# Optimization experiments

Measured on AMD Instinct MI355X. Metric: run time of the kernel, lower is better.

The kernel has to match this reference:

```python
import jax, jax.numpy as jnp
import numpy as np

EMBED_DIM = 1024
NUM_HEADS = 16
HEAD_DIM = EMBED_DIM // NUM_HEADS


def setup_inputs() -> dict:
    key = jax.random.key(0)
    ks = jax.random.split(key, 5)
    x = jax.random.normal(ks[0], (2, 2048, EMBED_DIM), dtype=jnp.float32)
    s_in = 1.0 / np.sqrt(EMBED_DIM)
    W_qkv = jax.random.uniform(ks[1], (EMBED_DIM, 3 * EMBED_DIM), minval=-s_in, maxval=s_in, dtype=jnp.float32)
    b_qkv = jax.random.uniform(ks[2], (3 * EMBED_DIM,), minval=-s_in, maxval=s_in, dtype=jnp.float32)
    W_out = jax.random.uniform(ks[3], (EMBED_DIM, EMBED_DIM), minval=-s_in, maxval=s_in, dtype=jnp.float32)
    b_out = jax.random.uniform(ks[4], (EMBED_DIM,), minval=-s_in, maxval=s_in, dtype=jnp.float32)
    return {"x": x, "W_qkv": W_qkv, "b_qkv": b_qkv, "W_out": W_out, "b_out": b_out}


def reference(x, W_qkv, b_qkv, W_out, b_out):
    B, S, D = x.shape
    H, Dh = NUM_HEADS, HEAD_DIM
    qkv = x @ W_qkv + b_qkv                       # [B, S, 3D]
    q, k, v = jnp.split(qkv, 3, axis=-1)
    # [B, S, D] -> [B, H, S, Dh]
    q = q.reshape(B, S, H, Dh).transpose(0, 2, 1, 3)
    k = k.reshape(B, S, H, Dh).transpose(0, 2, 1, 3)
    v = v.reshape(B, S, H, Dh).transpose(0, 2, 1, 3)
    scores = jnp.einsum('bhqd,bhkd->bhqk', q, k) / jnp.sqrt(jnp.float32(Dh))
    probs = jax.nn.softmax(scores, axis=-1)       # [B, H, S, S]
    attn = jnp.einsum('bhqk,bhkd->bhqd', probs, v)
    attn = attn.transpose(0, 2, 1, 3).reshape(B, S, D)
    return attn @ W_out + b_out
```

## Files before the change

kernel.cpp:

```cpp
#include <hip/hip_runtime.h>
#include <hip/hip_bf16.h>

#define DEV __device__ __forceinline__

typedef __bf16 bf16x8 __attribute__((ext_vector_type(8)));
typedef float f32x4 __attribute__((ext_vector_type(4)));
typedef float f32x16 __attribute__((ext_vector_type(16)));
using u16 = unsigned short;
using u32 = unsigned int;

static constexpr int S = 2048;
static constexpr int D = 1024;
static constexpr float SCQ = 0.125f * 1.44269504088896340736f;

DEV u16 f2bf(float f) {
  unsigned u = __builtin_bit_cast(unsigned, f);
  u += 0x7fffu + ((u >> 16) & 1u);
  return (u16)(u >> 16);
}
DEV u16 f2bfr(float f) {
  return (u16)((__builtin_bit_cast(u32, f) + 0x8000u) >> 16);
}
DEV u32 pk2(float a, float b) {
  u32 ua = __builtin_bit_cast(u32, a) + 0x8000u;
  u32 ub = __builtin_bit_cast(u32, b) + 0x8000u;
  return __builtin_amdgcn_perm(ub, ua, 0x07060302);
}

DEV void gl16(const u16* __restrict__ g, u16* l) {
  __builtin_amdgcn_global_load_lds((const __attribute__((address_space(1))) u32*)g,
                                   (__attribute__((address_space(3))) u32*)l, 16, 0, 0);
}

__global__ __launch_bounds__(256) void k_prep(const float* __restrict__ x, u16* __restrict__ Xb,
                                              const float* __restrict__ Wqkv, u16* __restrict__ WqkvT,
                                              const float* __restrict__ Wout, u16* __restrict__ WoutT) {
  __shared__ float t[32][33];
  const int bid = blockIdx.x;
  const int tid = threadIdx.x;
  if (bid < 4096) {
    const int i = bid * 256 + tid;
    const float4 v = reinterpret_cast<const float4*>(x)[i];
    ushort4 o;
    o.x = f2bf(v.x); o.y = f2bf(v.y); o.z = f2bf(v.z); o.w = f2bf(v.w);
    reinterpret_cast<ushort4*>(Xb)[i] = o;
    return;
  }
  const float* in;
  u16* out;
  int R, C, bx, by;
  if (bid < 4096 + 3072) {
    const int b = bid - 4096;
    in = Wqkv; out = WqkvT; R = 1024; C = 3072;
    bx = b % 96; by = b / 96;
  } else {
    const int b = bid - 7168;
    in = Wout; out = WoutT; R = 1024; C = 1024;
    bx = b & 31; by = b >> 5;
  }
  const int tx = tid & 31, ty = tid >> 5;
  const int c0 = bx * 32, r0 = by * 32;
  for (int i = ty; i < 32; i += 8)
    t[i][tx] = in[(size_t)(r0 + i) * C + c0 + tx];
  __syncthreads();
  for (int i = ty; i < 32; i += 8)
    out[(size_t)(c0 + i) * R + r0 + tx] = f2bf(t[tx][i]);
}

__global__ __launch_bounds__(256, 5) void k_gemm0(const u16* __restrict__ A, const u16* __restrict__ Bt,
                                                  const float* __restrict__ bias, int M, int N, int K,
                                                  u16* __restrict__ Qb, u16* __restrict__ Kb,
                                                  u16* __restrict__ Vt) {
  constexpr int TN = 128, NJ = 4;
  constexpr int ASZ = 2 * 128 * 32 * 2;
  __shared__ __align__(16) char smem[ASZ + 2 * TN * 32 * 2];
  auto As = reinterpret_cast<u16(*)[128][32]>(smem);
  auto Bs = reinterpret_cast<u16(*)[TN][32]>(smem + ASZ);
  auto LT = reinterpret_cast<u16(*)[136]>(smem);
  const int tid = threadIdx.x;
  const int lane = tid & 63, wave = tid >> 6;
  const int l15 = lane & 15, quad = lane >> 4;
  const int bid0 = blockIdx.x + 24 * blockIdx.y;
  const int bid = (bid0 & 7) * 96 + (bid0 >> 3);
  const int m0 = (bid / 24) * 128, n0 = (bid % 24) * TN;
  const int wm = (wave >> 1) * 64, wn = (wave & 1) * (TN / 2);
  const int lr = lane >> 2;
  const int lcs = ((((lane & 3) - (lane >> 3)) & 3)) * 8;
  const int sq = ((quad + (l15 >> 1)) & 3) * 8;

  f32x4 acc[4][NJ];
#pragma unroll
  for (int i = 0; i < 4; i++)
#pragma unroll
    for (int j = 0; j < NJ; j++) acc[i][j] = (f32x4){0.f, 0.f, 0.f, 0.f};

  const u16* Aw0 = &A[(size_t)(m0 + wave * 32 + lr) * K + lcs];
  const u16* Aw1 = &A[(size_t)(m0 + wave * 32 + 16 + lr) * K + lcs];
  const u16* Bw0 = &Bt[(size_t)(n0 + wave * 32 + lr) * K + lcs];
  const u16* Bw1 = &Bt[(size_t)(n0 + wave * 32 + 16 + lr) * K + lcs];

  gl16(Aw0, &As[0][wave * 32][0]);
  gl16(Aw1, &As[0][wave * 32 + 16][0]);
  gl16(Bw0, &Bs[0][wave * 32][0]);
  gl16(Bw1, &Bs[0][wave * 32 + 16][0]);

  int cur = 0;
#pragma unroll 2
  for (int kk = 0; kk < K; kk += 32, cur ^= 1) {
    __syncthreads();
    if (kk + 32 < K) {
      gl16(Aw0 + kk + 32, &As[cur ^ 1][wave * 32][0]);
      gl16(Aw1 + kk + 32, &As[cur ^ 1][wave * 32 + 16][0]);
      gl16(Bw0 + kk + 32, &Bs[cur ^ 1][wave * 32][0]);
      gl16(Bw1 + kk + 32, &Bs[cur ^ 1][wave * 32 + 16][0]);
    }
    bf16x8 af[4], bfv[NJ];
#pragma unroll
    for (int i = 0; i < 4; i++)
      af[i] = *reinterpret_cast<const bf16x8*>(&As[cur][wm + i * 16 + l15][sq]);
#pragma unroll
    for (int j = 0; j < NJ; j++)
      bfv[j] = *reinterpret_cast<const bf16x8*>(&Bs[cur][wn + j * 16 + l15][sq]);
#pragma unroll
    for (int i = 0; i < 4; i++)
#pragma unroll
      for (int j = 0; j < NJ; j++)
        acc[i][j] = __builtin_amdgcn_mfma_f32_16x16x32_bf16(af[i], bfv[j], acc[i][j], 0, 0, 0);
  }

  if (n0 >= 2048) {
    const int b = m0 >> 11, sbase = m0 & 2047;
#pragma unroll
    for (int p = 0; p < 2; p++) {
      __syncthreads();
      if ((wave & 1) == p) {
#pragma unroll
        for (int j = 0; j < NJ; j++) {
          const int n = n0 + wn + j * 16 + l15;
          const float vb = bias[n];
#pragma unroll
          for (int i = 0; i < 4; i++) {
            uint2 pw;
            pw.x = pk2(acc[i][j][0] + vb, acc[i][j][1] + vb);
            pw.y = pk2(acc[i][j][2] + vb, acc[i][j][3] + vb);
            *reinterpret_cast<uint2*>(&LT[j * 16 + l15][wm + i * 16 + quad * 4]) = pw;
          }
        }
      }
      __syncthreads();
      const int h = ((n0 - 2048) >> 6) + p;
      const int bh = b * 16 + h;
      const int nl = tid >> 2, cc = (tid & 3) * 32;
      u16* dst = &Vt[((size_t)bh * 64 + nl) * S + sbase + cc];
#pragma unroll
      for (int k = 0; k < 4; k++)
        reinterpret_cast<uint4*>(dst)[k] = *reinterpret_cast<const uint4*>(&LT[nl][cc + k * 8]);
    }
  } else {
#pragma unroll
    for (int i = 0; i < 4; i++) {
#pragma unroll
      for (int j = 0; j < NJ; j++) {
#pragma unroll
        for (int r = 0; r < 4; r++) {
          const int m = m0 + wm + i * 16 + quad * 4 + r;
          const int n = n0 + wn + j * 16 + l15;
          const float v = acc[i][j][r] + bias[n];
          const int h = (n >> 6) & 15, dh = n & 63;
          const int b = m >> 11, s = m & 2047;
          const int bh = b * 16 + h;
          if (n < 1024) Qb[((size_t)bh * S + s) * 64 + dh] = f2bfr(v * SCQ);
          else          Kb[((size_t)bh * S + s) * 64 + dh] = f2bfr(v);
        }
      }
    }
  }
}

__global__ __launch_bounds__(256, 4) void k_gemm2(const u16* __restrict__ A, const u16* __restrict__ Bt,
                                                  const float* __restrict__ bias, float* __restrict__ outF) {
  constexpr int K = 1024, N = 1024;
  __shared__ __align__(16) u16 As[2][64][64];
  __shared__ __align__(16) u16 Bs[2][64][64];
  const int tid = threadIdx.x;
  const int lane = tid & 63, wave = tid >> 6;
  const int l15 = lane & 15, quad = lane >> 4;
  const int bid0 = blockIdx.x + 16 * blockIdx.y;
  const int bid = (bid0 & 7) * 128 + (bid0 >> 3);
  const int m0 = (bid >> 4) * 64, n0 = (bid & 15) * 64;
  const int wm = (wave >> 1) * 32, wn = (wave & 1) * 32;
  const int srow = lane >> 3;
  const int scol = ((lane & 7) ^ srow) * 8;

  f32x4 acc[2][2];
#pragma unroll
  for (int i = 0; i < 2; i++)
#pragma unroll
    for (int j = 0; j < 2; j++) acc[i][j] = (f32x4){0.f, 0.f, 0.f, 0.f};

  const u16* Ap[2];
  const u16* Bp[2];
#pragma unroll
  for (int c = 0; c < 2; c++) {
    Ap[c] = &A[(size_t)(m0 + wave * 16 + c * 8 + srow) * K + scol];
    Bp[c] = &Bt[(size_t)(n0 + wave * 16 + c * 8 + srow) * K + scol];
  }

#pragma unroll
  for (int c = 0; c < 2; c++) {
    gl16(Ap[c], &As[0][wave * 16 + c * 8][0]);
    gl16(Bp[c], &Bs[0][wave * 16 + c * 8][0]);
  }

  int cur = 0;
#pragma unroll 2
  for (int kk = 0; kk < K; kk += 64, cur ^= 1) {
    __syncthreads();
    if (kk + 64 < K) {
#pragma unroll
      for (int c = 0; c < 2; c++) {
        gl16(Ap[c] + kk + 64, &As[cur ^ 1][wave * 16 + c * 8][0]);
        gl16(Bp[c] + kk + 64, &Bs[cur ^ 1][wave * 16 + c * 8][0]);
      }
    }
#pragma unroll
    for (int ks = 0; ks < 2; ks++) {
      const int sc = ((ks * 4 + quad) ^ (l15 & 7)) * 8;
      bf16x8 af[2], bfv[2];
#pragma unroll
      for (int i = 0; i < 2; i++)
        af[i] = *reinterpret_cast<const bf16x8*>(&As[cur][wm + i * 16 + l15][sc]);
#pragma unroll
      for (int j = 0; j < 2; j++)
        bfv[j] = *reinterpret_cast<const bf16x8*>(&Bs[cur][wn + j * 16 + l15][sc]);
#pragma unroll
      for (int i = 0; i < 2; i++)
#pragma unroll
        for (int j = 0; j < 2; j++)
          acc[i][j] = __builtin_amdgcn_mfma_f32_16x16x32_bf16(af[i], bfv[j], acc[i][j], 0, 0, 0);
    }
  }

#pragma unroll
  for (int i = 0; i < 2; i++)
#pragma unroll
    for (int j = 0; j < 2; j++)
#pragma unroll
      for (int r = 0; r < 4; r++) {
        const int m = m0 + wm + i * 16 + quad * 4 + r;
        const int n = n0 + wn + j * 16 + l15;
        outF[(size_t)m * N + n] = acc[i][j][r] + bias[n];
      }
}

__global__ __launch_bounds__(256, 2) void k_attn(const u16* __restrict__ Qb,
                                                 const u16* __restrict__ Kb,
                                                 const u16* __restrict__ Vt,
                                                 u16* __restrict__ attnB) {
  __shared__ u16 Ks[64][72];
  __shared__ u16 Vs[64][72];
  __shared__ u16 Pl[4][32][72];
  const int tid = threadIdx.x;
  const int lane = tid & 63, wave = tid >> 6;
  const int l31 = lane & 31, hi = lane >> 5;
  const int bid0 = blockIdx.x + 16 * blockIdx.y;
  const int bid = (bid0 & 7) * 64 + (bid0 >> 3);
  const int bh = bid >> 4;
  const int q0 = (bid & 15) * 128;
  const u16* Qh = Qb + (size_t)bh * S * 64;
  const u16* Kh = Kb + (size_t)bh * S * 64;
  const u16* Vh = Vt + (size_t)bh * 64 * S;
  const int qrow = q0 + wave * 32 + l31;
  bf16x8 qf[4];
#pragma unroll
  for (int f = 0; f < 4; f++)
    qf[f] = *reinterpret_cast<const bf16x8*>(&Qh[(size_t)qrow * 64 + f * 16 + hi * 8]);

  const int r0 = tid >> 3, c0 = (tid & 7) * 8;

  float li = 0.f;
  f32x16 o0, o1;
#pragma unroll
  for (int r = 0; r < 16; r++) { o0[r] = 0.f; o1[r] = 0.f; }

  uint4 pk0 = *reinterpret_cast<const uint4*>(&Kh[(size_t)r0 * 64 + c0]);
  uint4 pk1 = *reinterpret_cast<const uint4*>(&Kh[(size_t)(r0 + 32) * 64 + c0]);
  uint4 pv0 = *reinterpret_cast<const uint4*>(&Vh[(size_t)r0 * S + c0]);
  uint4 pv1 = *reinterpret_cast<const uint4*>(&Vh[(size_t)(r0 + 32) * S + c0]);

  for (int kb = 0; kb < S / 64; kb++) {
    __syncthreads();
    *reinterpret_cast<uint4*>(&Ks[r0][c0]) = pk0;
    *reinterpret_cast<uint4*>(&Ks[r0 + 32][c0]) = pk1;
    *reinterpret_cast<uint4*>(&Vs[r0][c0]) = pv0;
    *reinterpret_cast<uint4*>(&Vs[r0 + 32][c0]) = pv1;
    __syncthreads();
    if (kb + 1 < S / 64) {
      const u16* Kn = Kh + (size_t)(kb + 1) * 64 * 64;
      pk0 = *reinterpret_cast<const uint4*>(&Kn[(size_t)r0 * 64 + c0]);
      pk1 = *reinterpret_cast<const uint4*>(&Kn[(size_t)(r0 + 32) * 64 + c0]);
      pv0 = *reinterpret_cast<const uint4*>(&Vh[(size_t)r0 * S + (kb + 1) * 64 + c0]);
      pv1 = *reinterpret_cast<const uint4*>(&Vh[(size_t)(r0 + 32) * S + (kb + 1) * 64 + c0]);
    }
    f32x16 z[2];
    __builtin_amdgcn_s_setprio(1);
#pragma unroll
    for (int kt = 0; kt < 2; kt++) {
#pragma unroll
      for (int r = 0; r < 16; r++) z[kt][r] = 0.f;
#pragma unroll
      for (int f = 0; f < 4; f++) {
        const bf16x8 a = *reinterpret_cast<const bf16x8*>(&Ks[kt * 32 + l31][f * 16 + hi * 8]);
        z[kt] = __builtin_amdgcn_mfma_f32_32x32x16_bf16(a, qf[f], z[kt], 0, 0, 0);
      }
    }
    __builtin_amdgcn_s_setprio(0);
    float s0 = 0.f, s1 = 0.f, s2 = 0.f, s3 = 0.f;
#pragma unroll
    for (int kt = 0; kt < 2; kt++)
#pragma unroll
      for (int r = 0; r < 16; r++) {
        const float p = __builtin_amdgcn_exp2f(z[kt][r]);
        z[kt][r] = p;
        if ((r & 3) == 0) s0 += p; else if ((r & 3) == 1) s1 += p;
        else if ((r & 3) == 2) s2 += p; else s3 += p;
      }
    li += (s0 + s1) + (s2 + s3);
#pragma unroll
    for (int kt = 0; kt < 2; kt++)
#pragma unroll
      for (int g = 0; g < 4; g++) {
        uint2 pw;
        pw.x = pk2(z[kt][g * 4 + 0], z[kt][g * 4 + 1]);
        pw.y = pk2(z[kt][g * 4 + 2], z[kt][g * 4 + 3]);
        *reinterpret_cast<uint2*>(&Pl[wave][l31][kt * 32 + g * 8 + hi * 4]) = pw;
      }
    __builtin_amdgcn_s_setprio(1);
#pragma unroll
    for (int f = 0; f < 4; f++) {
      const bf16x8 bp = *reinterpret_cast<const bf16x8*>(&Pl[wave][l31][f * 16 + hi * 8]);
      const bf16x8 av0 = *reinterpret_cast<const bf16x8*>(&Vs[l31][f * 16 + hi * 8]);
      const bf16x8 av1 = *reinterpret_cast<const bf16x8*>(&Vs[32 + l31][f * 16 + hi * 8]);
      o0 = __builtin_amdgcn_mfma_f32_32x32x16_bf16(av0, bp, o0, 0, 0, 0);
      o1 = __builtin_amdgcn_mfma_f32_32x32x16_bf16(av1, bp, o1, 0, 0, 0);
    }
    __builtin_amdgcn_s_setprio(0);
  }
  li += __shfl_xor(li, 32);
  const float inv = 1.f / li;
#pragma unroll
  for (int dt = 0; dt < 2; dt++) {
    const f32x16& od = dt ? o1 : o0;
#pragma unroll
    for (int g = 0; g < 4; g++) {
      uint2 ow;
      ow.x = pk2(od[g * 4 + 0] * inv, od[g * 4 + 1] * inv);
      ow.y = pk2(od[g * 4 + 2] * inv, od[g * 4 + 3] * inv);
      *reinterpret_cast<uint2*>(&Pl[wave][l31][dt * 32 + g * 8 + hi * 4]) = ow;
    }
  }
  const int b = bh >> 4, h = bh & 15;
  const int mbase = b * S + q0 + wave * 32;
  const int qr = lane >> 1, ch = (lane & 1) * 32;
  u16* dst = &attnB[(size_t)(mbase + qr) * D + h * 64 + ch];
#pragma unroll
  for (int c = 0; c < 4; c++)
    reinterpret_cast<uint4*>(dst)[c] = *reinterpret_cast<const uint4*>(&Pl[wave][qr][ch + c * 8]);
}

extern "C" void kernel_launch(void* const* d_in, const int* in_sizes, int n_in,
                              void* d_out, int out_size, void* d_ws, size_t ws_size,
                              hipStream_t stream) {
  const float* x = (const float*)d_in[0];
  const float* Wqkv = (const float*)d_in[1];
  const float* bqkv = (const float*)d_in[2];
  const float* Wout = (const float*)d_in[3];
  const float* bout = (const float*)d_in[4];
  float* out = (float*)d_out;

  char* p = (char*)d_ws;
  u16* Xb = (u16*)p;    p += (size_t)4096 * 1024 * 2;
  u16* WqkvT = (u16*)p; p += (size_t)3072 * 1024 * 2;
  u16* WoutT = (u16*)p; p += (size_t)1024 * 1024 * 2;
  u16* Qb = (u16*)p;    p += (size_t)32 * 2048 * 64 * 2;
  u16* Kb = (u16*)p;    p += (size_t)32 * 2048 * 64 * 2;
  u16* Vt = (u16*)p;    p += (size_t)32 * 64 * 2048 * 2;
  u16* attnB = (u16*)p; p += (size_t)4096 * 1024 * 2;

  k_prep<<<4096 + 3072 + 1024, 256, 0, stream>>>(x, Xb, Wqkv, WqkvT, Wout, WoutT);
  k_gemm0<<<dim3(3072 / 128, 4096 / 128), 256, 0, stream>>>(
      Xb, WqkvT, bqkv, 4096, 3072, 1024, Qb, Kb, Vt);
  k_attn<<<dim3(2048 / 128, 32), 256, 0, stream>>>(Qb, Kb, Vt, attnB);
  k_gemm2<<<dim3(1024 / 64, 4096 / 64), 256, 0, stream>>>(attnB, WoutT, bout, out);
}
```

Baseline: 188.7 us.

## Split-K output GEMM with larger tiles, separate reduction, and register-based P handoff in attention

The output projection now uses 128x128 tiles with a two-way split-K, writing fp32 partials into reused workspace, and a new kernel sums them and adds the bias. This is meant to raise per-block reuse while keeping enough blocks to fill the GPU. Separately, the attention kernel no longer stages P through LDS. It rearranges the packed bf16 probabilities across lanes with v_permlane32_swap and feeds them straight to the PV MFMA, saving LDS round trips. The cost is an extra launch and about 32MB of partial-sum traffic, and the workspace buffers are reordered so the partials can alias the Xb and WqkvT region.

```diff
diff --git a/kernel.cpp b/kernel.cpp
--- a/kernel.cpp
+++ b/kernel.cpp
@@ -177,80 +177,91 @@
   }
 }
 
-__global__ __launch_bounds__(256, 4) void k_gemm2(const u16* __restrict__ A, const u16* __restrict__ Bt,
-                                                  const float* __restrict__ bias, float* __restrict__ outF) {
-  constexpr int K = 1024, N = 1024;
-  __shared__ __align__(16) u16 As[2][64][64];
-  __shared__ __align__(16) u16 Bs[2][64][64];
+__global__ __launch_bounds__(256, 5) void k_gemm2(const u16* __restrict__ A, const u16* __restrict__ Bt,
+                                                  float* __restrict__ Pp) {
+  constexpr int K = 1024, N = 1024, KH = 512;
+  constexpr int ASZ = 2 * 128 * 32 * 2;
+  __shared__ __align__(16) char smem[2 * ASZ];
+  auto As = reinterpret_cast<u16(*)[128][32]>(smem);
+  auto Bs = reinterpret_cast<u16(*)[128][32]>(smem + ASZ);
   const int tid = threadIdx.x;
   const int lane = tid & 63, wave = tid >> 6;
   const int l15 = lane & 15, quad = lane >> 4;
-  const int bid0 = blockIdx.x + 16 * blockIdx.y;
-  const int bid = (bid0 & 7) * 128 + (bid0 >> 3);
-  const int m0 = (bid >> 4) * 64, n0 = (bid & 15) * 64;
-  const int wm = (wave >> 1) * 32, wn = (wave & 1) * 32;
-  const int srow = lane >> 3;
-  const int scol = ((lane & 7) ^ srow) * 8;
-
-  f32x4 acc[2][2];
-#pragma unroll
-  for (int i = 0; i < 2; i++)
-#pragma unroll
-    for (int j = 0; j < 2; j++) acc[i][j] = (f32x4){0.f, 0.f, 0.f, 0.f};
-
-  const u16* Ap[2];
-  const u16* Bp[2];
-#pragma unroll
-  for (int c = 0; c < 2; c++) {
-    Ap[c] = &A[(size_t)(m0 + wave * 16 + c * 8 + srow) * K + scol];
-    Bp[c] = &Bt[(size_t)(n0 + wave * 16 + c * 8 + srow) * K + scol];
-  }
-
-#pragma unroll
-  for (int c = 0; c < 2; c++) {
-    gl16(Ap[c], &As[0][wave * 16 + c * 8][0]);
-    gl16(Bp[c], &Bs[0][wave * 16 + c * 8][0]);
-  }
+  const int bid0 = blockIdx.x;
+  const int bid = (bid0 & 7) * 64 + (bid0 >> 3);
+  const int ks = bid >> 8, rem = bid & 255;
+  const int m0 = (rem >> 3) * 128, n0 = (rem & 7) * 128;
+  const int koff = ks * KH;
+  const int wm = (wave >> 1) * 64, wn = (wave & 1) * 64;
+  const int lr = lane >> 2;
+  const int lcs = ((((lane & 3) - (lane >> 3)) & 3)) * 8;
+  const int sq = ((quad + (l15 >> 1)) & 3) * 8;
+
+  f32x4 acc[4][4];
+#pragma unroll
+  for (int i = 0; i < 4; i++)
+#pragma unroll
+    for (int j = 0; j < 4; j++) acc[i][j] = (f32x4){0.f, 0.f, 0.f, 0.f};
+
+  const u16* Aw0 = &A[(size_t)(m0 + wave * 32 + lr) * K + koff + lcs];
+  const u16* Aw1 = &A[(size_t)(m0 + wave * 32 + 16 + lr) * K + koff + lcs];
+  const u16* Bw0 = &Bt[(size_t)(n0 + wave * 32 + lr) * K + koff + lcs];
+  const u16* Bw1 = &Bt[(size_t)(n0 + wave * 32 + 16 + lr) * K + koff + lcs];
+
+  gl16(Aw0, &As[0][wave * 32][0]);
+  gl16(Aw1, &As[0][wave * 32 + 16][0]);
+  gl16(Bw0, &Bs[0][wave * 32][0]);
+  gl16(Bw1, &Bs[0][wave * 32 + 16][0]);
 
   int cur = 0;
 #pragma unroll 2
-  for (int kk = 0; kk < K; kk += 64, cur ^= 1) {
+  for (int kk = 0; kk < KH; kk += 32, cur ^= 1) {
     __syncthreads();
-    if (kk + 64 < K) {
-#pragma unroll
-      for (int c = 0; c < 2; c++) {
-        gl16(Ap[c] + kk + 64, &As[cur ^ 1][wave * 16 + c * 8][0]);
-        gl16(Bp[c] + kk + 64, &Bs[cur ^ 1][wave * 16 + c * 8][0]);
-      }
-    }
-#pragma unroll
-    for (int ks = 0; ks < 2; ks++) {
-      const int sc = ((ks * 4 + quad) ^ (l15 & 7)) * 8;
-      bf16x8 af[2], bfv[2];
-#pragma unroll
-      for (int i = 0; i < 2; i++)
-        af[i] = *reinterpret_cast<const bf16x8*>(&As[cur][wm + i * 16 + l15][sc]);
-#pragma unroll
-      for (int j = 0; j < 2; j++)
-        bfv[j] = *reinterpret_cast<const bf16x8*>(&Bs[cur][wn + j * 16 + l15][sc]);
-#pragma unroll
-      for (int i = 0; i < 2; i++)
-#pragma unroll
-        for (int j = 0; j < 2; j++)
-          acc[i][j] = __builtin_amdgcn_mfma_f32_16x16x32_bf16(af[i], bfv[j], acc[i][j], 0, 0, 0);
-    }
-  }
-
-#pragma unroll
-  for (int i = 0; i < 2; i++)
-#pragma unroll
-    for (int j = 0; j < 2; j++)
+    if (kk + 32 < KH) {
+      gl16(Aw0 + kk + 32, &As[cur ^ 1][wave * 32][0]);
+      gl16(Aw1 + kk + 32, &As[cur ^ 1][wave * 32 + 16][0]);
+      gl16(Bw0 + kk + 32, &Bs[cur ^ 1][wave * 32][0]);
+      gl16(Bw1 + kk + 32, &Bs[cur ^ 1][wave * 32 + 16][0]);
+    }
+    bf16x8 af[4], bfv[4];
+#pragma unroll
+    for (int i = 0; i < 4; i++)
+      af[i] = *reinterpret_cast<const bf16x8*>(&As[cur][wm + i * 16 + l15][sq]);
+#pragma unroll
+    for (int j = 0; j < 4; j++)
+      bfv[j] = *reinterpret_cast<const bf16x8*>(&Bs[cur][wn + j * 16 + l15][sq]);
+#pragma unroll
+    for (int i = 0; i < 4; i++)
+#pragma unroll
+      for (int j = 0; j < 4; j++)
+        acc[i][j] = __builtin_amdgcn_mfma_f32_16x16x32_bf16(af[i], bfv[j], acc[i][j], 0, 0, 0);
+  }
+
+  float* Pq = Pp + (size_t)ks * 4096 * 1024;
+#pragma unroll
+  for (int i = 0; i < 4; i++)
+#pragma unroll
+    for (int j = 0; j < 4; j++)
 #pragma unroll
       for (int r = 0; r < 4; r++) {
         const int m = m0 + wm + i * 16 + quad * 4 + r;
         const int n = n0 + wn + j * 16 + l15;
-        outF[(size_t)m * N + n] = acc[i][j][r] + bias[n];
-      }
+        Pq[(size_t)m * N + n] = acc[i][j][r];
+      }
+}
+
+__global__ __launch_bounds__(256) void k_red(const float* __restrict__ p0, const float* __restrict__ p1,
+                                             const float* __restrict__ bias, float* __restrict__ out) {
+  const int i = blockIdx.x * 256 + threadIdx.x;
+  const float4 a = reinterpret_cast<const float4*>(p0)[i];
+  const float4 b = reinterpret_cast<const float4*>(p1)[i];
+  const float4 c = reinterpret_cast<const float4*>(bias)[i & 255];
+  float4 o;
+  o.x = a.x + b.x + c.x;
+  o.y = a.y + b.y + c.y;
+  o.z = a.z + b.z + c.z;
+  o.w = a.w + b.w + c.w;
+  reinterpret_cast<float4*>(out)[i] = o;
 }
 
 __global__ __launch_bounds__(256, 2) void k_attn(const u16* __restrict__ Qb,
@@ -326,23 +337,26 @@
         else if ((r & 3) == 2) s2 += p; else s3 += p;
       }
     li += (s0 + s1) + (s2 + s3);
-#pragma unroll
-    for (int kt = 0; kt < 2; kt++)
-#pragma unroll
-      for (int g = 0; g < 4; g++) {
-        uint2 pw;
-        pw.x = pk2(z[kt][g * 4 + 0], z[kt][g * 4 + 1]);
-        pw.y = pk2(z[kt][g * 4 + 2], z[kt][g * 4 + 3]);
-        *reinterpret_cast<uint2*>(&Pl[wave][l31][kt * 32 + g * 8 + hi * 4]) = pw;
-      }
     __builtin_amdgcn_s_setprio(1);
 #pragma unroll
-    for (int f = 0; f < 4; f++) {
-      const bf16x8 bp = *reinterpret_cast<const bf16x8*>(&Pl[wave][l31][f * 16 + hi * 8]);
-      const bf16x8 av0 = *reinterpret_cast<const bf16x8*>(&Vs[l31][f * 16 + hi * 8]);
-      const bf16x8 av1 = *reinterpret_cast<const bf16x8*>(&Vs[32 + l31][f * 16 + hi * 8]);
-      o0 = __builtin_amdgcn_mfma_f32_32x32x16_bf16(av0, bp, o0, 0, 0, 0);
-      o1 = __builtin_amdgcn_mfma_f32_32x32x16_bf16(av1, bp, o1, 0, 0, 0);
+    for (int kt = 0; kt < 2; kt++) {
+#pragma unroll
+      for (int s = 0; s < 2; s++) {
+        u32 w0 = pk2(z[kt][s * 8 + 0], z[kt][s * 8 + 1]);
+        u32 w2 = pk2(z[kt][s * 8 + 4], z[kt][s * 8 + 5]);
+        asm("v_permlane32_swap_b32 %0, %1" : "+v"(w0), "+v"(w2));
+        u32 w1 = pk2(z[kt][s * 8 + 2], z[kt][s * 8 + 3]);
+        u32 w3 = pk2(z[kt][s * 8 + 6], z[kt][s * 8 + 7]);
+        asm("v_permlane32_swap_b32 %0, %1" : "+v"(w1), "+v"(w3));
+        uint4 wv;
+        wv.x = w0; wv.y = w1; wv.z = w2; wv.w = w3;
+        const bf16x8 bp = __builtin_bit_cast(bf16x8, wv);
+        const int f = kt * 2 + s;
+        const bf16x8 av0 = *reinterpret_cast<const bf16x8*>(&Vs[l31][f * 16 + hi * 8]);
+        const bf16x8 av1 = *reinterpret_cast<const bf16x8*>(&Vs[32 + l31][f * 16 + hi * 8]);
+        o0 = __builtin_amdgcn_mfma_f32_32x32x16_bf16(av0, bp, o0, 0, 0, 0);
+        o1 = __builtin_amdgcn_mfma_f32_32x32x16_bf16(av1, bp, o1, 0, 0, 0);
+      }
     }
     __builtin_amdgcn_s_setprio(0);
   }
@@ -379,17 +393,19 @@
   float* out = (float*)d_out;
 
   char* p = (char*)d_ws;
+  u16* WoutT = (u16*)p; p += (size_t)1024 * 1024 * 2;
+  u16* attnB = (u16*)p; p += (size_t)4096 * 1024 * 2;
   u16* Xb = (u16*)p;    p += (size_t)4096 * 1024 * 2;
   u16* WqkvT = (u16*)p; p += (size_t)3072 * 1024 * 2;
-  u16* WoutT = (u16*)p; p += (size_t)1024 * 1024 * 2;
+  u16* Vt = (u16*)p;    p += (size_t)32 * 64 * 2048 * 2;
   u16* Qb = (u16*)p;    p += (size_t)32 * 2048 * 64 * 2;
   u16* Kb = (u16*)p;    p += (size_t)32 * 2048 * 64 * 2;
-  u16* Vt = (u16*)p;    p += (size_t)32 * 64 * 2048 * 2;
-  u16* attnB = (u16*)p; p += (size_t)4096 * 1024 * 2;
+  float* Pp = (float*)Xb;
 
   k_prep<<<4096 + 3072 + 1024, 256, 0, stream>>>(x, Xb, Wqkv, WqkvT, Wout, WoutT);
   k_gemm0<<<dim3(3072 / 128, 4096 / 128), 256, 0, stream>>>(
       Xb, WqkvT, bqkv, 4096, 3072, 1024, Qb, Kb, Vt);
   k_attn<<<dim3(2048 / 128, 32), 256, 0, stream>>>(Qb, Kb, Vt, attnB);
-  k_gemm2<<<dim3(1024 / 64, 4096 / 64), 256, 0, stream>>>(attnB, WoutT, bout, out);
-}
+  k_gemm2<<<512, 256, 0, stream>>>(attnB, WoutT, Pp);
+  k_red<<<4096, 256, 0, stream>>>(Pp, Pp + (size_t)4096 * 1024, bout, out);
+}
```

Measured after the change: 198.4 us. 5.1% more time.
